# Kernel optimization log

Hardware: AMD Instinct MI355X
Metric: run time of the kernel (lower is better)

## Reference

```python
import jax, jax.numpy as jnp
import numpy as np

H = 1024      # hidden_size
NH = 16       # attention heads
DH = H // NH  # head dim
B, S = 4, 2048
EPS = 1e-12


def setup_inputs() -> dict:
    key = jax.random.key(0)
    ks = jax.random.split(key, 9)
    sc = 1.0 / np.sqrt(H)
    inp = {
        "input_tensor": jax.random.normal(ks[0], (B, S, H), dtype=jnp.float32),
        "Wq": jax.random.normal(ks[1], (H, H), dtype=jnp.float32) * sc,
        "bq": jnp.zeros((H,), jnp.float32),
        "Wk": jax.random.normal(ks[2], (H, H), dtype=jnp.float32) * sc,
        "bk": jnp.zeros((H,), jnp.float32),
        "Wv": jax.random.normal(ks[3], (H, H), dtype=jnp.float32) * sc,
        "bv": jnp.zeros((H,), jnp.float32),
        "Wo": jax.random.normal(ks[4], (H, H), dtype=jnp.float32) * sc,
        "bo": jnp.zeros((H,), jnp.float32),
        "gamma": jnp.ones((H,), jnp.float32),
        "beta": jnp.zeros((H,), jnp.float32),
    }
    return inp


def _heads(x):
    # [B,S,H] -> [B,NH,S,DH]
    b, s, _ = x.shape
    return x.reshape(b, s, NH, DH).transpose(0, 2, 1, 3)


def reference(input_tensor, Wq, bq, Wk, bk, Wv, bv, Wo, bo, gamma, beta):
    q = _heads(input_tensor @ Wq.T + bq)
    k = _heads(input_tensor @ Wk.T + bk)
    v = _heads(input_tensor @ Wv.T + bv)
    scores = jnp.einsum("bhqd,bhkd->bhqk", q, k) / jnp.sqrt(jnp.float32(DH))
    probs = jax.nn.softmax(scores, axis=-1)  # dropout p=0 -> identity
    ctx = jnp.einsum("bhqk,bhkd->bhqd", probs, v)
    ctx = ctx.transpose(0, 2, 1, 3).reshape(input_tensor.shape)  # [B,S,H]
    h = ctx @ Wo.T + bo
    x = h + input_tensor
    u = jnp.mean(x, axis=-1, keepdims=True)
    s2 = jnp.mean((x - u) ** 2, axis=-1, keepdims=True)
    xn = (x - u) / jnp.sqrt(s2 + EPS)
    return gamma * xn + beta
```

## Files before the change

### kernel.cpp

```cpp
#include <hip/hip_runtime.h>
#include <math.h>

#define H   1024
#define NH  16
#define DH  64
#define BB  4
#define SS  2048
#define M_ROWS (BB*SS)
#define EPS 1e-12f
#define QSCALE 0.18033688011112042f

typedef __attribute__((ext_vector_type(4))) float f32x4;
typedef __attribute__((ext_vector_type(8))) short bf16x8;
typedef const __attribute__((address_space(1))) void* as1cvp;
typedef __attribute__((address_space(3))) void*       as3vp;

__device__ __forceinline__ unsigned short f2bf(float f) {
    union { float f; unsigned u; } x; x.f = f;
    unsigned r = x.u + 0x7fffu + ((x.u >> 16) & 1u);
    return (unsigned short)(r >> 16);
}
__device__ __forceinline__ unsigned pk2bf(float lo, float hi) {
    return __builtin_amdgcn_perm(__float_as_uint(hi), __float_as_uint(lo), 0x07060302u);
}

__global__ __launch_bounds__(256)
void cvt_all(const float4* __restrict__ x,
             const float4* __restrict__ wq, const float4* __restrict__ wk,
             const float4* __restrict__ wv, const float4* __restrict__ wo,
             ushort4* __restrict__ xb, ushort4* __restrict__ wqb,
             ushort4* __restrict__ wkb, ushort4* __restrict__ wvb,
             ushort4* __restrict__ wob)
{
    int id = blockIdx.x * 256 + threadIdx.x;
    const float4* src; ushort4* dst; int off;
    if (id < 2097152) { src = x; dst = xb; off = id; }
    else {
        int t = id - 2097152, wsel = t >> 18;
        off = t & 262143;
        src = wsel == 0 ? wq : wsel == 1 ? wk : wsel == 2 ? wv : wo;
        dst = wsel == 0 ? wqb : wsel == 1 ? wkb : wsel == 2 ? wvb : wob;
    }
    float4 v = src[off];
    ushort4 o; o.x = f2bf(v.x); o.y = f2bf(v.y); o.z = f2bf(v.z); o.w = f2bf(v.w);
    dst[off] = o;
}

__device__ __forceinline__ void gemm_core_128(const ushort* __restrict__ A,
                                              const ushort* __restrict__ Wt,
                                              ushort* AsP, ushort* BsP,
                                              int row0, int col0, int K,
                                              f32x4 (&acc)[4][4])
{
    const int tid = threadIdx.x, lane = tid & 63, w = tid >> 6;
    const int wr = w >> 1, wc = w & 1, l15 = lane & 15, quad = lane >> 4;
    const int lr = lane >> 2, kc = lane & 3;
    const int qs  = kc ^ ((lr >> 1) & 3);
    const int qsw = (quad ^ ((l15 >> 1) & 3)) * 8;

    const __attribute__((address_space(1))) ushort* gA =
        (const __attribute__((address_space(1))) ushort*)A;
    const __attribute__((address_space(1))) ushort* gB =
        (const __attribute__((address_space(1))) ushort*)Wt;
    __attribute__((address_space(3))) ushort* lA = (__attribute__((address_space(3))) ushort*)AsP;
    __attribute__((address_space(3))) ushort* lB = (__attribute__((address_space(3))) ushort*)BsP;

    const int ra = (w * 2) * 16 + lr;
    const int rb = ra + 16;

    for (int k0 = 0; k0 < K; k0 += 32) {
        __builtin_amdgcn_global_load_lds((as1cvp)(gA + (size_t)(row0 + ra) * K + k0 + qs * 8),
                                         (as3vp)(lA + (w * 2 + 0) * 512), 16, 0, 0);
        __builtin_amdgcn_global_load_lds((as1cvp)(gA + (size_t)(row0 + rb) * K + k0 + qs * 8),
                                         (as3vp)(lA + (w * 2 + 1) * 512), 16, 0, 0);
        __builtin_amdgcn_global_load_lds((as1cvp)(gB + (size_t)(col0 + ra) * K + k0 + qs * 8),
                                         (as3vp)(lB + (w * 2 + 0) * 512), 16, 0, 0);
        __builtin_amdgcn_global_load_lds((as1cvp)(gB + (size_t)(col0 + rb) * K + k0 + qs * 8),
                                         (as3vp)(lB + (w * 2 + 1) * 512), 16, 0, 0);
        __syncthreads();
        bf16x8 af[4], bfr[4];
        #pragma unroll
        for (int rt = 0; rt < 4; ++rt)
            af[rt] = *(const bf16x8*)&AsP[(wr * 64 + rt * 16 + l15) * 32 + qsw];
        #pragma unroll
        for (int ct = 0; ct < 4; ++ct)
            bfr[ct] = *(const bf16x8*)&BsP[(wc * 64 + ct * 16 + l15) * 32 + qsw];
        #pragma unroll
        for (int rt = 0; rt < 4; ++rt)
            #pragma unroll
            for (int ct = 0; ct < 4; ++ct)
                acc[rt][ct] = __builtin_amdgcn_mfma_f32_16x16x32_bf16(af[rt], bfr[ct], acc[rt][ct], 0, 0, 0);
        __syncthreads();
    }
}

__global__ __launch_bounds__(256)
void qkv_gemm(const ushort* __restrict__ xb,
              const ushort* __restrict__ Wqb, const ushort* __restrict__ Wkb,
              const ushort* __restrict__ Wvb,
              const float* __restrict__ bq, const float* __restrict__ bk,
              const float* __restrict__ bv,
              ushort* __restrict__ Qb, ushort* __restrict__ Kb, ushort* __restrict__ Vt)
{
    __shared__ ushort As[128 * 32];
    __shared__ ushort Bs[128 * 32];
    const int z = blockIdx.z;
    const ushort* Wt  = z == 0 ? Wqb : z == 1 ? Wkb : Wvb;
    const float* bias = z == 0 ? bq  : z == 1 ? bk  : bv;
    const int row0 = blockIdx.y * 128, col0 = blockIdx.x * 128;

    f32x4 acc[4][4];
    #pragma unroll
    for (int i = 0; i < 4; ++i)
        #pragma unroll
        for (int j = 0; j < 4; ++j)
            acc[i][j] = (f32x4){0.f, 0.f, 0.f, 0.f};

    gemm_core_128(xb, Wt, As, Bs, row0, col0, H, acc);

    const int tid = threadIdx.x, lane = tid & 63, w = tid >> 6;
    const int wr = w >> 1, wc = w & 1, l15 = lane & 15, quad = lane >> 4;

    #pragma unroll
    for (int rt = 0; rt < 4; ++rt) {
        const int r0g = row0 + wr * 64 + rt * 16 + quad * 4;
        #pragma unroll
        for (int ct = 0; ct < 4; ++ct) {
            const int c = col0 + wc * 64 + ct * 16 + l15;
            const float bs = bias[c];
            if (z == 0) {
                #pragma unroll
                for (int i = 0; i < 4; ++i)
                    Qb[(size_t)(r0g + i) * H + c] = f2bf((acc[rt][ct][i] + bs) * QSCALE);
            } else if (z == 1) {
                #pragma unroll
                for (int i = 0; i < 4; ++i)
                    Kb[(size_t)(r0g + i) * H + c] = f2bf(acc[rt][ct][i] + bs);
            } else {
                const int bb = r0g >> 11, s0 = r0g & 2047;
                const int hh = c >> 6, dd = c & 63;
                ushort4 o;
                o.x = f2bf(acc[rt][ct][0] + bs);
                o.y = f2bf(acc[rt][ct][1] + bs);
                o.z = f2bf(acc[rt][ct][2] + bs);
                o.w = f2bf(acc[rt][ct][3] + bs);
                *(ushort4*)&Vt[(((size_t)(bb * 16 + hh) * 64 + dd) << 11) + s0] = o;
            }
        }
    }
}

__global__ __launch_bounds__(256)
void oproj_gemm(const ushort* __restrict__ ctxb, const ushort* __restrict__ Wob,
                const float* __restrict__ bo, const float* __restrict__ res,
                float* __restrict__ Xr)
{
    __shared__ ushort As[128 * 32];
    __shared__ ushort Bs[128 * 32];
    const int row0 = blockIdx.y * 128, col0 = blockIdx.x * 128;

    f32x4 acc[4][4];
    #pragma unroll
    for (int i = 0; i < 4; ++i)
        #pragma unroll
        for (int j = 0; j < 4; ++j)
            acc[i][j] = (f32x4){0.f, 0.f, 0.f, 0.f};

    gemm_core_128(ctxb, Wob, As, Bs, row0, col0, H, acc);

    const int tid = threadIdx.x, lane = tid & 63, w = tid >> 6;
    const int wr = w >> 1, wc = w & 1, l15 = lane & 15, quad = lane >> 4;

    #pragma unroll
    for (int rt = 0; rt < 4; ++rt) {
        const int r0g = row0 + wr * 64 + rt * 16 + quad * 4;
        #pragma unroll
        for (int ct = 0; ct < 4; ++ct) {
            const int c = col0 + wc * 64 + ct * 16 + l15;
            const float bs = bo[c];
            #pragma unroll
            for (int i = 0; i < 4; ++i) {
                size_t idx = (size_t)(r0g + i) * H + c;
                Xr[idx] = acc[rt][ct][i] + bs + res[idx];
            }
        }
    }
}

#define KTILE 64
#define NKT (SS / KTILE)

__global__ __launch_bounds__(256, 5)
void flash_attn_mfma(const ushort* __restrict__ Qb, const ushort* __restrict__ Kb,
                     const ushort* __restrict__ Vt, ushort* __restrict__ ctx)
{
    __shared__ __align__(16) ushort Ks[2][KTILE * 64];
    __shared__ __align__(16) ushort Vs[2][64 * KTILE];

    const int tid  = threadIdx.x;
    const int lane = tid & 63;
    const int w    = tid >> 6;
    const int l15  = lane & 15, quad = lane >> 4;
    const int bh   = blockIdx.x & 63;
    const int qt   = blockIdx.x >> 6;
    const int b    = bh >> 4, h = bh & 15;
    const int row0 = qt * 64 + w * 16;
    const size_t qk_base = (size_t)(b * SS) * H + h * DH;
    const size_t vt_base = (size_t)((b * 16 + h) * 64) * SS;

    const __attribute__((address_space(1))) ushort* gK =
        (const __attribute__((address_space(1))) ushort*)Kb;
    const __attribute__((address_space(1))) ushort* gV =
        (const __attribute__((address_space(1))) ushort*)Vt;

    const int srow = lane >> 3;
    const int c8   = lane & 7;
    const int sck0 = c8 ^ ((srow & 3) | (((w * 2 + 0) & 1) << 2));
    const int sck1 = c8 ^ ((srow & 3) | (((w * 2 + 1) & 1) << 2));

    const int fL = (l15 & 3) | (((l15 >> 2) & 1) << 2);
    const int fV = (l15 & 3) | (((l15 >> 3) & 1) << 2);
    const int rA = 8 * (l15 >> 2) + (l15 & 3);
    int kOff0[4], kOff1[4], vOff0[4], vOff1[4];
    #pragma unroll
    for (int ct = 0; ct < 4; ++ct) {
        const int r = rA + (ct & 1) * 4 + (ct >> 1) * 32;
        kOff0[ct] = r * 64 + ((quad ^ fL) * 8);
        kOff1[ct] = r * 64 + (((4 | quad) ^ fL) * 8);
    }
    #pragma unroll
    for (int dt = 0; dt < 4; ++dt) {
        const int rv = dt * 16 + l15;
        vOff0[dt] = rv * 64 + ((quad ^ fV) * 8);
        vOff1[dt] = rv * 64 + (((4 | quad) ^ fV) * 8);
    }

    const bf16x8 aq0 = *(const bf16x8*)&Qb[qk_base + (size_t)(row0 + l15) * H + quad * 8];
    const bf16x8 aq1 = *(const bf16x8*)&Qb[qk_base + (size_t)(row0 + l15) * H + 32 + quad * 8];

    float lp = 0.f;
    f32x4 o[4];
    #pragma unroll
    for (int dt = 0; dt < 4; ++dt) o[dt] = (f32x4){0.f, 0.f, 0.f, 0.f};

    const __attribute__((address_space(1))) ushort* gK0 =
        gK + qk_base + (size_t)(w * 16 + srow) * H;
    const __attribute__((address_space(1))) ushort* gV0 =
        gV + vt_base + (size_t)(w * 16 + srow) * SS;

    __builtin_amdgcn_global_load_lds((as1cvp)(gK0 + sck0 * 8),
                                     (as3vp)(&Ks[0][(w * 16) * 64]), 16, 0, 0);
    __builtin_amdgcn_global_load_lds((as1cvp)(gK0 + (size_t)8 * H + sck1 * 8),
                                     (as3vp)(&Ks[0][(w * 16 + 8) * 64]), 16, 0, 0);
    __builtin_amdgcn_global_load_lds((as1cvp)(gV0 + sck0 * 8),
                                     (as3vp)(&Vs[0][(w * 16) * 64]), 16, 0, 0);
    __builtin_amdgcn_global_load_lds((as1cvp)(gV0 + (size_t)8 * SS + sck1 * 8),
                                     (as3vp)(&Vs[0][(w * 16 + 8) * 64]), 16, 0, 0);

    for (int kt = 0; kt < NKT; ++kt) {
        __syncthreads();

        if (kt + 1 < NKT) {
            const int j0 = (kt + 1) * KTILE;
            const int nb = (kt + 1) & 1;
            __builtin_amdgcn_global_load_lds((as1cvp)(gK0 + (size_t)j0 * H + sck0 * 8),
                                             (as3vp)(&Ks[nb][(w * 16) * 64]), 16, 0, 0);
            __builtin_amdgcn_global_load_lds((as1cvp)(gK0 + (size_t)(j0 + 8) * H + sck1 * 8),
                                             (as3vp)(&Ks[nb][(w * 16 + 8) * 64]), 16, 0, 0);
            __builtin_amdgcn_global_load_lds((as1cvp)(gV0 + j0 + sck0 * 8),
                                             (as3vp)(&Vs[nb][(w * 16) * 64]), 16, 0, 0);
            __builtin_amdgcn_global_load_lds((as1cvp)(gV0 + (size_t)8 * SS + j0 + sck1 * 8),
                                             (as3vp)(&Vs[nb][(w * 16 + 8) * 64]), 16, 0, 0);
        }

        const ushort* Ktile = Ks[kt & 1];
        const ushort* Vtile = Vs[kt & 1];

        f32x4 s[4];
        __builtin_amdgcn_s_setprio(1);
        #pragma unroll
        for (int ct = 0; ct < 4; ++ct) {
            const bf16x8 k0 = *(const bf16x8*)&Ktile[kOff0[ct]];
            const bf16x8 k1 = *(const bf16x8*)&Ktile[kOff1[ct]];
            f32x4 z = (f32x4){0.f, 0.f, 0.f, 0.f};
            z = __builtin_amdgcn_mfma_f32_16x16x32_bf16(k0, aq0, z, 0, 0, 0);
            z = __builtin_amdgcn_mfma_f32_16x16x32_bf16(k1, aq1, z, 0, 0, 0);
            s[ct] = z;
        }
        __builtin_amdgcn_s_setprio(0);

        unsigned pw[8];
        #pragma unroll
        for (int ct = 0; ct < 4; ++ct) {
            const float p0 = __builtin_amdgcn_exp2f(s[ct][0]);
            const float p1 = __builtin_amdgcn_exp2f(s[ct][1]);
            const float p2 = __builtin_amdgcn_exp2f(s[ct][2]);
            const float p3 = __builtin_amdgcn_exp2f(s[ct][3]);
            lp += (p0 + p1) + (p2 + p3);
            pw[ct * 2 + 0] = pk2bf(p0, p1);
            pw[ct * 2 + 1] = pk2bf(p2, p3);
        }
        union { unsigned u[4]; bf16x8 v; } A0, A1;
        A0.u[0] = pw[0]; A0.u[1] = pw[1]; A0.u[2] = pw[2]; A0.u[3] = pw[3];
        A1.u[0] = pw[4]; A1.u[1] = pw[5]; A1.u[2] = pw[6]; A1.u[3] = pw[7];

        __builtin_amdgcn_s_setprio(1);
        #pragma unroll
        for (int dt = 0; dt < 4; ++dt) {
            const bf16x8 v0 = *(const bf16x8*)&Vtile[vOff0[dt]];
            const bf16x8 v1 = *(const bf16x8*)&Vtile[vOff1[dt]];
            o[dt] = __builtin_amdgcn_mfma_f32_16x16x32_bf16(A0.v, v0, o[dt], 0, 0, 0);
            o[dt] = __builtin_amdgcn_mfma_f32_16x16x32_bf16(A1.v, v1, o[dt], 0, 0, 0);
        }
        __builtin_amdgcn_s_setprio(0);
    }

    float lr = lp;
    lr += __shfl_xor(lr, 16);
    lr += __shfl_xor(lr, 32);
    #pragma unroll
    for (int i = 0; i < 4; ++i) {
        const float inv = 1.f / __shfl(lr, quad * 4 + i);
        const int r = row0 + quad * 4 + i;
        #pragma unroll
        for (int dt = 0; dt < 4; ++dt)
            ctx[qk_base + (size_t)r * H + dt * 16 + l15] = f2bf(o[dt][i] * inv);
    }
}

__global__ __launch_bounds__(256)
void ln_kernel(const float* __restrict__ Xr, const float* __restrict__ gamma,
               const float* __restrict__ beta, float* __restrict__ out)
{
    __shared__ float red[256], red2[256];
    const int row = blockIdx.x;
    const int tid = threadIdx.x;
    const float4 v = ((const float4*)(Xr + (size_t)row * H))[tid];
    float s  = v.x + v.y + v.z + v.w;
    float ss = v.x * v.x + v.y * v.y + v.z * v.z + v.w * v.w;
    red[tid] = s; red2[tid] = ss;
    __syncthreads();
    for (int st = 128; st > 0; st >>= 1) {
        if (tid < st) { red[tid] += red[tid + st]; red2[tid] += red2[tid + st]; }
        __syncthreads();
    }
    const float mean = red[0] * (1.f / H);
    const float var  = red2[0] * (1.f / H) - mean * mean;
    const float rstd = rsqrtf(var + EPS);
    const float4 g  = ((const float4*)gamma)[tid];
    const float4 be = ((const float4*)beta)[tid];
    float4 o;
    o.x = g.x * (v.x - mean) * rstd + be.x;
    o.y = g.y * (v.y - mean) * rstd + be.y;
    o.z = g.z * (v.z - mean) * rstd + be.z;
    o.w = g.w * (v.w - mean) * rstd + be.w;
    ((float4*)(out + (size_t)row * H))[tid] = o;
}

extern "C" void kernel_launch(void* const* d_in, const int* in_sizes, int n_in,
                              void* d_out, int out_size, void* d_ws, size_t ws_size,
                              hipStream_t stream)
{
    const float* x     = (const float*)d_in[0];
    const float* Wq    = (const float*)d_in[1];
    const float* bq    = (const float*)d_in[2];
    const float* Wk    = (const float*)d_in[3];
    const float* bk    = (const float*)d_in[4];
    const float* Wv    = (const float*)d_in[5];
    const float* bv    = (const float*)d_in[6];
    const float* Wo    = (const float*)d_in[7];
    const float* bo    = (const float*)d_in[8];
    const float* gamma = (const float*)d_in[9];
    const float* beta  = (const float*)d_in[10];

    char* ws = (char*)d_ws;
    ushort* xb  = (ushort*)(ws);
    ushort* Wqb = (ushort*)(ws + (size_t)(16 << 20));
    ushort* Wkb = (ushort*)(ws + (size_t)(18 << 20));
    ushort* Wvb = (ushort*)(ws + (size_t)(20 << 20));
    ushort* Wob = (ushort*)(ws + (size_t)(22 << 20));
    ushort* Qb  = (ushort*)(ws + (size_t)(24 << 20));
    ushort* Kb  = (ushort*)(ws + (size_t)(40 << 20));
    ushort* Vt  = (ushort*)(ws + (size_t)(56 << 20));
    float*  Xr  = (float*) (ws + (size_t)(40 << 20));

    cvt_all<<<12288, 256, 0, stream>>>((const float4*)x, (const float4*)Wq, (const float4*)Wk,
                                       (const float4*)Wv, (const float4*)Wo,
                                       (ushort4*)xb, (ushort4*)Wqb, (ushort4*)Wkb,
                                       (ushort4*)Wvb, (ushort4*)Wob);

    qkv_gemm<<<dim3(H / 128, M_ROWS / 128, 3), 256, 0, stream>>>(
        xb, Wqb, Wkb, Wvb, bq, bk, bv, Qb, Kb, Vt);

    flash_attn_mfma<<<BB * NH * (SS / 64), 256, 0, stream>>>(Qb, Kb, Vt, Qb );

    oproj_gemm<<<dim3(H / 128, M_ROWS / 128), 256, 0, stream>>>(Qb, Wob, bo, x, Xr);

    ln_kernel<<<M_ROWS, 256, 0, stream>>>(Xr, gamma, beta, (float*)d_out);
}
```

Before: 304.3 us.

## Double-buffer GEMM LDS tiles and compute softmax row sums via MFMA

```diff
diff --git a/kernel.cpp b/kernel.cpp
--- a/kernel.cpp
+++ b/kernel.cpp
@@ -14,6 +14,8 @@
 typedef __attribute__((ext_vector_type(8))) short bf16x8;
 typedef const __attribute__((address_space(1))) void* as1cvp;
 typedef __attribute__((address_space(3))) void*       as3vp;
+typedef const __attribute__((address_space(1))) ushort* as1u;
+typedef __attribute__((address_space(3))) ushort*       as3u;
 
 __device__ __forceinline__ unsigned short f2bf(float f) {
     union { float f; unsigned u; } x; x.f = f;
@@ -48,7 +50,8 @@
 
 __device__ __forceinline__ void gemm_core_128(const ushort* __restrict__ A,
                                               const ushort* __restrict__ Wt,
-                                              ushort* AsP, ushort* BsP,
+                                              ushort* As0P, ushort* As1P,
+                                              ushort* Bs0P, ushort* Bs1P,
                                               int row0, int col0, int K,
                                               f32x4 (&acc)[4][4])
 {
@@ -58,39 +61,53 @@
     const int qs  = kc ^ ((lr >> 1) & 3);
     const int qsw = (quad ^ ((l15 >> 1) & 3)) * 8;
 
-    const __attribute__((address_space(1))) ushort* gA =
-        (const __attribute__((address_space(1))) ushort*)A;
-    const __attribute__((address_space(1))) ushort* gB =
-        (const __attribute__((address_space(1))) ushort*)Wt;
-    __attribute__((address_space(3))) ushort* lA = (__attribute__((address_space(3))) ushort*)AsP;
-    __attribute__((address_space(3))) ushort* lB = (__attribute__((address_space(3))) ushort*)BsP;
+    const as1u gA = (as1u)A;
+    const as1u gB = (as1u)Wt;
+    as3u lA0 = (as3u)As0P, lA1 = (as3u)As1P;
+    as3u lB0 = (as3u)Bs0P, lB1 = (as3u)Bs1P;
 
     const int ra = (w * 2) * 16 + lr;
     const int rb = ra + 16;
-
-    for (int k0 = 0; k0 < K; k0 += 32) {
-        __builtin_amdgcn_global_load_lds((as1cvp)(gA + (size_t)(row0 + ra) * K + k0 + qs * 8),
-                                         (as3vp)(lA + (w * 2 + 0) * 512), 16, 0, 0);
-        __builtin_amdgcn_global_load_lds((as1cvp)(gA + (size_t)(row0 + rb) * K + k0 + qs * 8),
-                                         (as3vp)(lA + (w * 2 + 1) * 512), 16, 0, 0);
-        __builtin_amdgcn_global_load_lds((as1cvp)(gB + (size_t)(col0 + ra) * K + k0 + qs * 8),
-                                         (as3vp)(lB + (w * 2 + 0) * 512), 16, 0, 0);
-        __builtin_amdgcn_global_load_lds((as1cvp)(gB + (size_t)(col0 + rb) * K + k0 + qs * 8),
-                                         (as3vp)(lB + (w * 2 + 1) * 512), 16, 0, 0);
-        __syncthreads();
+    const size_t gAr0 = (size_t)(row0 + ra) * K + qs * 8;
+    const size_t gAr1 = (size_t)(row0 + rb) * K + qs * 8;
+    const size_t gBr0 = (size_t)(col0 + ra) * K + qs * 8;
+    const size_t gBr1 = (size_t)(col0 + rb) * K + qs * 8;
+
+    auto STAGE0 = [&](int k0) {
+        __builtin_amdgcn_global_load_lds((as1cvp)(gA + gAr0 + k0), (as3vp)(lA0 + (w * 2 + 0) * 512), 16, 0, 0);
+        __builtin_amdgcn_global_load_lds((as1cvp)(gA + gAr1 + k0), (as3vp)(lA0 + (w * 2 + 1) * 512), 16, 0, 0);
+        __builtin_amdgcn_global_load_lds((as1cvp)(gB + gBr0 + k0), (as3vp)(lB0 + (w * 2 + 0) * 512), 16, 0, 0);
+        __builtin_amdgcn_global_load_lds((as1cvp)(gB + gBr1 + k0), (as3vp)(lB0 + (w * 2 + 1) * 512), 16, 0, 0);
+    };
+    auto STAGE1 = [&](int k0) {
+        __builtin_amdgcn_global_load_lds((as1cvp)(gA + gAr0 + k0), (as3vp)(lA1 + (w * 2 + 0) * 512), 16, 0, 0);
+        __builtin_amdgcn_global_load_lds((as1cvp)(gA + gAr1 + k0), (as3vp)(lA1 + (w * 2 + 1) * 512), 16, 0, 0);
+        __builtin_amdgcn_global_load_lds((as1cvp)(gB + gBr0 + k0), (as3vp)(lB1 + (w * 2 + 0) * 512), 16, 0, 0);
+        __builtin_amdgcn_global_load_lds((as1cvp)(gB + gBr1 + k0), (as3vp)(lB1 + (w * 2 + 1) * 512), 16, 0, 0);
+    };
+    auto COMPUTE = [&](const ushort* Asrc, const ushort* Bsrc) {
         bf16x8 af[4], bfr[4];
         #pragma unroll
         for (int rt = 0; rt < 4; ++rt)
-            af[rt] = *(const bf16x8*)&AsP[(wr * 64 + rt * 16 + l15) * 32 + qsw];
+            af[rt] = *(const bf16x8*)&Asrc[(wr * 64 + rt * 16 + l15) * 32 + qsw];
         #pragma unroll
         for (int ct = 0; ct < 4; ++ct)
-            bfr[ct] = *(const bf16x8*)&BsP[(wc * 64 + ct * 16 + l15) * 32 + qsw];
+            bfr[ct] = *(const bf16x8*)&Bsrc[(wc * 64 + ct * 16 + l15) * 32 + qsw];
         #pragma unroll
         for (int rt = 0; rt < 4; ++rt)
             #pragma unroll
             for (int ct = 0; ct < 4; ++ct)
                 acc[rt][ct] = __builtin_amdgcn_mfma_f32_16x16x32_bf16(af[rt], bfr[ct], acc[rt][ct], 0, 0, 0);
+    };
+
+    STAGE0(0);
+    for (int k0 = 0; k0 < K; k0 += 64) {
         __syncthreads();
+        if (k0 + 32 < K) STAGE1(k0 + 32);
+        COMPUTE(As0P, Bs0P);
+        __syncthreads();
+        if (k0 + 64 < K) STAGE0(k0 + 64);
+        if (k0 + 32 < K) COMPUTE(As1P, Bs1P);
     }
 }
 
@@ -102,8 +119,8 @@
               const float* __restrict__ bv,
               ushort* __restrict__ Qb, ushort* __restrict__ Kb, ushort* __restrict__ Vt)
 {
-    __shared__ ushort As[128 * 32];
-    __shared__ ushort Bs[128 * 32];
+    __shared__ ushort As[2][128 * 32];
+    __shared__ ushort Bs[2][128 * 32];
     const int z = blockIdx.z;
     const ushort* Wt  = z == 0 ? Wqb : z == 1 ? Wkb : Wvb;
     const float* bias = z == 0 ? bq  : z == 1 ? bk  : bv;
@@ -116,7 +133,7 @@
         for (int j = 0; j < 4; ++j)
             acc[i][j] = (f32x4){0.f, 0.f, 0.f, 0.f};
 
-    gemm_core_128(xb, Wt, As, Bs, row0, col0, H, acc);
+    gemm_core_128(xb, Wt, &As[0][0], &As[1][0], &Bs[0][0], &Bs[1][0], row0, col0, H, acc);
 
     const int tid = threadIdx.x, lane = tid & 63, w = tid >> 6;
     const int wr = w >> 1, wc = w & 1, l15 = lane & 15, quad = lane >> 4;
@@ -155,8 +172,8 @@
                 const float* __restrict__ bo, const float* __restrict__ res,
                 float* __restrict__ Xr)
 {
-    __shared__ ushort As[128 * 32];
-    __shared__ ushort Bs[128 * 32];
+    __shared__ ushort As[2][128 * 32];
+    __shared__ ushort Bs[2][128 * 32];
     const int row0 = blockIdx.y * 128, col0 = blockIdx.x * 128;
 
     f32x4 acc[4][4];
@@ -166,7 +183,7 @@
         for (int j = 0; j < 4; ++j)
             acc[i][j] = (f32x4){0.f, 0.f, 0.f, 0.f};
 
-    gemm_core_128(ctxb, Wob, As, Bs, row0, col0, H, acc);
+    gemm_core_128(ctxb, Wob, &As[0][0], &As[1][0], &Bs[0][0], &Bs[1][0], row0, col0, H, acc);
 
     const int tid = threadIdx.x, lane = tid & 63, w = tid >> 6;
     const int wr = w >> 1, wc = w & 1, l15 = lane & 15, quad = lane >> 4;
@@ -208,10 +225,8 @@
     const size_t qk_base = (size_t)(b * SS) * H + h * DH;
     const size_t vt_base = (size_t)((b * 16 + h) * 64) * SS;
 
-    const __attribute__((address_space(1))) ushort* gK =
-        (const __attribute__((address_space(1))) ushort*)Kb;
-    const __attribute__((address_space(1))) ushort* gV =
-        (const __attribute__((address_space(1))) ushort*)Vt;
+    const as1u gK = (const as1u)Kb;
+    const as1u gV = (const as1u)Vt;
 
     const int srow = lane >> 3;
     const int c8   = lane & 7;
@@ -238,15 +253,17 @@
     const bf16x8 aq0 = *(const bf16x8*)&Qb[qk_base + (size_t)(row0 + l15) * H + quad * 8];
     const bf16x8 aq1 = *(const bf16x8*)&Qb[qk_base + (size_t)(row0 + l15) * H + 32 + quad * 8];
 
-    float lp = 0.f;
+    union { unsigned u[4]; bf16x8 v; } ONES;
+    #pragma unroll
+    for (int i = 0; i < 4; ++i) ONES.u[i] = 0x3F803F80u;
+
+    f32x4 acc_l = (f32x4){0.f, 0.f, 0.f, 0.f};
     f32x4 o[4];
     #pragma unroll
     for (int dt = 0; dt < 4; ++dt) o[dt] = (f32x4){0.f, 0.f, 0.f, 0.f};
 
-    const __attribute__((address_space(1))) ushort* gK0 =
-        gK + qk_base + (size_t)(w * 16 + srow) * H;
-    const __attribute__((address_space(1))) ushort* gV0 =
-        gV + vt_base + (size_t)(w * 16 + srow) * SS;
+    const as1u gK0 = gK + qk_base + (size_t)(w * 16 + srow) * H;
+    const as1u gV0 = gV + vt_base + (size_t)(w * 16 + srow) * SS;
 
     __builtin_amdgcn_global_load_lds((as1cvp)(gK0 + sck0 * 8),
                                      (as3vp)(&Ks[0][(w * 16) * 64]), 16, 0, 0);
@@ -296,7 +313,6 @@
             const float p1 = __builtin_amdgcn_exp2f(s[ct][1]);
             const float p2 = __builtin_amdgcn_exp2f(s[ct][2]);
             const float p3 = __builtin_amdgcn_exp2f(s[ct][3]);
-            lp += (p0 + p1) + (p2 + p3);
             pw[ct * 2 + 0] = pk2bf(p0, p1);
             pw[ct * 2 + 1] = pk2bf(p2, p3);
         }
@@ -305,6 +321,8 @@
         A1.u[0] = pw[4]; A1.u[1] = pw[5]; A1.u[2] = pw[6]; A1.u[3] = pw[7];
 
         __builtin_amdgcn_s_setprio(1);
+        acc_l = __builtin_amdgcn_mfma_f32_16x16x32_bf16(A0.v, ONES.v, acc_l, 0, 0, 0);
+        acc_l = __builtin_amdgcn_mfma_f32_16x16x32_bf16(A1.v, ONES.v, acc_l, 0, 0, 0);
         #pragma unroll
         for (int dt = 0; dt < 4; ++dt) {
             const bf16x8 v0 = *(const bf16x8*)&Vtile[vOff0[dt]];
@@ -315,12 +333,9 @@
         __builtin_amdgcn_s_setprio(0);
     }
 
-    float lr = lp;
-    lr += __shfl_xor(lr, 16);
-    lr += __shfl_xor(lr, 32);
     #pragma unroll
     for (int i = 0; i < 4; ++i) {
-        const float inv = 1.f / __shfl(lr, quad * 4 + i);
+        const float inv = 1.f / acc_l[i];
         const int r = row0 + quad * 4 + i;
         #pragma unroll
         for (int dt = 0; dt < 4; ++dt)
```

Result: slower. 322.0 us (+5.8%).
